# Kernel optimization log

Measured on AMD Instinct MI355X. Metric: run time of the kernel, lower is better.

The kernel has to match this reference:

```python
import jax, jax.numpy as jnp
import numpy as np
import math

P = 256   # state_dim
H = 1024  # hidden_dim
B = 8     # batch
L = 4096  # sequence length
R_MIN, R_MAX, THETA_MAX = 0.9, 0.999, math.pi


def _map_theta_to_A(thetas, G_diag, steps):
    cos_t = jnp.cos(thetas)
    tan_sq = jnp.tan(thetas) ** 2
    sqrt_term = 4.0 * jnp.sqrt(steps ** 4 / cos_t ** 2 + steps ** 5 * G_diag / cos_t ** 2)
    common = steps ** 2 * (-4.0 - 2.0 * steps * G_diag - 4.0 * tan_sq - 2.0 * steps * G_diag * tan_sq)
    denom = 2.0 * steps ** 4 * (1.0 + tan_sq)
    A_plus = (sqrt_term - common) / denom
    A_minus = (-sqrt_term - common) / denom
    return jnp.where(thetas > math.pi / 2, A_plus, A_minus)


def setup_inputs() -> dict:
    key = jax.random.key(0)
    k1, k2, k3, k4, k5, k6, k7 = jax.random.split(key, 7)
    x = jax.random.normal(k1, (B, L, H), dtype=jnp.float32)
    steps_raw = 0.5 * jax.random.normal(k2, (P,), dtype=jnp.float32)
    steps = jax.nn.sigmoid(steps_raw)
    mags = jnp.sqrt(jax.random.uniform(k3, (P,)) * (R_MAX ** 2 - R_MIN ** 2) + R_MIN ** 2)
    G_raw = (1.0 - mags ** 2) / (steps * mags ** 2)
    theta = jax.random.uniform(k4, (P,)) * THETA_MAX
    A_raw = _map_theta_to_A(theta, jax.nn.relu(G_raw), steps)
    std_b = 1.0 / math.sqrt(H)
    B_mat = jax.random.uniform(k5, (P, H, 2), minval=-std_b, maxval=std_b, dtype=jnp.float32)
    std_c = 1.0 / math.sqrt(P)
    C_mat = jax.random.uniform(k6, (H, P, 2), minval=-std_c, maxval=std_c, dtype=jnp.float32)
    D_vec = jax.random.normal(k7, (H,), dtype=jnp.float32)
    return {"input_sequence": x, "steps_raw": steps_raw, "G_raw": G_raw,
            "A_raw": A_raw, "B_mat": B_mat, "C_mat": C_mat, "D_vec": D_vec}


def _binary_operator(q_i, q_j):
    """Compose (M, F) pairs: (Mj@Mi, Mj@Fi + Fj); M flattened as [M11,M12,M21,M22] (4P)."""
    A_i, b_i = q_i
    A_j, b_j = q_j
    iA, iB, iC, iD = jnp.split(A_i, 4, axis=-1)
    jA, jB, jC, jD = jnp.split(A_j, 4, axis=-1)
    A_new = jnp.concatenate([jA * iA + jB * iC, jA * iB + jB * iD,
                             jC * iA + jD * iC, jC * iB + jD * iD], axis=-1)
    b_i1, b_i2 = jnp.split(b_i, 2, axis=-2)  # (..., P, 2) each
    new_b1 = jA[..., None] * b_i1 + jB[..., None] * b_i2
    new_b2 = jC[..., None] * b_i1 + jD[..., None] * b_i2
    return A_new, jnp.concatenate([new_b1, new_b2], axis=-2) + b_j


def _forward(x, steps_raw, G_raw, A_raw, B_mat, C_mat, D_vec):
    steps = jax.nn.sigmoid(steps_raw)          # (P,)
    G_diag = jax.nn.relu(G_raw)
    A_diag = jax.nn.relu(A_raw)

    Bu = jnp.einsum('blh,pht->blpt', x, B_mat)  # (B, L, P, 2)

    S = 1.0 + steps * G_diag                    # (P,)
    alpha = steps ** 2 * A_diag / S
    alpha = 1.99 * jnp.tanh(alpha / 1.99)
    M = jnp.concatenate([1.0 / S, -alpha / steps, steps / S, 1.0 - alpha])  # (4P,)
    M_exp = jnp.broadcast_to(M, (x.shape[0], x.shape[1], 4 * steps.shape[0]))

    step_b = steps[None, None, :, None]
    S_b = S[None, None, :, None]
    F1 = step_b * (1.0 / S_b) * Bu
    F2 = step_b ** 2 * (1.0 / S_b) * Bu
    F_mat = jnp.concatenate([F1, F2], axis=-2)  # (B, L, 2P, 2)

    _, xs = jax.lax.associative_scan(_binary_operator, (M_exp, F_mat), axis=1)
    ys = xs[..., steps.shape[0]:, :]            # (B, L, P, 2) -- the x-states

    Cy = jnp.einsum('blpt,hpt->blht', ys, C_mat)  # (B, L, H, 2)
    return Cy[..., 0] - Cy[..., 1] + x * D_vec


def reference(input_sequence, steps_raw, G_raw, A_raw, B_mat, C_mat, D_vec):
    return _forward(input_sequence, steps_raw, G_raw, A_raw, B_mat, C_mat, D_vec)
```

## Files before the change

### kernel.cpp

```cpp
#include <hip/hip_runtime.h>
#include <math.h>
#include <stdint.h>

#define PCH 256
#define HD  1024
#define BB  8
#define LL  4096
#define NN  512
#define MROWS (BB*LL)
#define NCH 64
#define TCH 64

typedef __bf16 bf16x8 __attribute__((ext_vector_type(8)));
typedef float  f32x4  __attribute__((ext_vector_type(4)));
typedef short  s16x8  __attribute__((ext_vector_type(8)));

#define OFFB_W1    ((size_t)0)
#define OFFB_C2    (OFFB_W1  + (size_t)NN*HD*2)
#define OFFB_CST   (OFFB_C2  + (size_t)HD*NN*2)
#define OFFB_BU    (OFFB_CST + (size_t)16384)
#define OFFB_YS    (OFFB_BU  + (size_t)MROWS*NN*2)
#define OFFB_ZEND  (OFFB_YS  + (size_t)MROWS*NN*2)
#define OFFB_CARRY (OFFB_ZEND + (size_t)BB*NCH*2*NN*4)

__device__ __forceinline__ short f2bf(float f) {
    union { float f; uint32_t u; } v; v.f = f;
    uint32_t r = v.u + 0x7FFFu + ((v.u >> 16) & 1u);
    return (short)(r >> 16);
}
__device__ __forceinline__ float bf2f(unsigned short u) {
    union { uint32_t u; float f; } v; v.u = ((uint32_t)u) << 16;
    return v.f;
}

__global__ void prep_consts(const float* __restrict__ steps_raw,
                            const float* __restrict__ G_raw,
                            const float* __restrict__ A_raw,
                            float* __restrict__ cst) {
    int p = threadIdx.x;
    if (p >= PCH) return;
    float steps = 1.0f / (1.0f + expf(-steps_raw[p]));
    float G = fmaxf(G_raw[p], 0.0f);
    float A = fmaxf(A_raw[p], 0.0f);
    float S = 1.0f + steps * G;
    float alpha = steps * steps * A / S;
    alpha = 1.99f * tanhf(alpha / 1.99f);
    float m11 = 1.0f / S;
    float m12 = -alpha / steps;
    float m21 = steps / S;
    float m22 = 1.0f - alpha;
    float c1 = steps / S;
    float c2 = steps * steps / S;
    float a = 1.f, b = 0.f, c = 0.f, d = 1.f;
    for (int i = 0; i < TCH; ++i) {
        float na = m11*a + m12*c;
        float nb = m11*b + m12*d;
        float nc = m21*a + m22*c;
        float nd = m21*b + m22*d;
        a = na; b = nb; c = nc; d = nd;
    }
    cst[0*PCH+p] = m11; cst[1*PCH+p] = m12; cst[2*PCH+p] = m21; cst[3*PCH+p] = m22;
    cst[4*PCH+p] = c1;  cst[5*PCH+p] = c2;
    cst[6*PCH+p] = a;   cst[7*PCH+p] = b;   cst[8*PCH+p] = c;   cst[9*PCH+p] = d;
}

__global__ void prep_w(const float* __restrict__ B_mat,
                       const float* __restrict__ C_mat,
                       short* __restrict__ W1t,
                       short* __restrict__ C2t) {
    int idx = blockIdx.x * blockDim.x + threadIdx.x;
    if (idx >= HD * NN) return;
    {
        int n = idx >> 10;
        int h = idx & (HD - 1);
        int p = n >> 1, t = n & 1;
        W1t[idx] = f2bf(B_mat[(size_t)p * HD * 2 + (size_t)h * 2 + t]);
    }
    {
        int h = idx >> 9;
        int n = idx & (NN - 1);
        int p = n >> 1, t = n & 1;
        float sgn = (t == 0) ? 1.0f : -1.0f;
        C2t[idx] = f2bf(sgn * C_mat[(size_t)h * PCH * 2 + (size_t)p * 2 + t]);
    }
}

template <int K, int N, bool A_F32, bool OUT_BF16, bool EPI>
__global__ __launch_bounds__(256, 3)
void gemm128(const void* __restrict__ Aop, const short* __restrict__ Bt,
             void* __restrict__ Cout, const float* __restrict__ xres,
             const float* __restrict__ Dv) {
    __shared__ alignas(16) char smem[32768];
    constexpr int GX = N / 128;
    const int nwg = gridDim.x;
    const int cpx = nwg >> 3;
    const int bid = blockIdx.x;
    const int wg = (bid & 7) * cpx + (bid >> 3);
    const int by = wg / GX, bx = wg % GX;
    const int m0 = by * 128, n0 = bx * 128;

    const int tid = threadIdx.x;
    const int lane = tid & 63, w = tid >> 6;
    const int wm = w >> 1, wn = w & 1;
    const int g = lane >> 4, r16 = lane & 15;

    const short* Abf  = (const short*)Aop;
    const float* Af32 = (const float*)Aop;

    auto stageB = [&](int buf, int k0) {
        #pragma unroll
        for (int s = 0; s < 2; ++s) {
            int c = tid + s * 256;
            int row = c >> 2, q = c & 3;
            int gq = q ^ ((row >> 1) & 3);
            const short* sb = Bt + (size_t)(n0 + row) * K + k0 + gq * 8;
            __builtin_amdgcn_global_load_lds(
                (const __attribute__((address_space(1))) void*)sb,
                (__attribute__((address_space(3))) void*)(smem + buf * 16384 + 8192 + c * 16),
                16, 0, 0);
        }
    };
    auto stageAbf = [&](int buf, int k0) {
        #pragma unroll
        for (int s = 0; s < 2; ++s) {
            int c = tid + s * 256;
            int row = c >> 2, q = c & 3;
            int gq = q ^ ((row >> 1) & 3);
            const short* sa = Abf + (size_t)(m0 + row) * K + k0 + gq * 8;
            __builtin_amdgcn_global_load_lds(
                (const __attribute__((address_space(1))) void*)sa,
                (__attribute__((address_space(3))) void*)(smem + buf * 16384 + c * 16),
                16, 0, 0);
        }
    };
    f32x4 av0, av1, av2, av3;
    auto loadAf32 = [&](int k0) {
        {
            int c = tid;
            int row = c >> 2, q = c & 3;
            const f32x4* px = (const f32x4*)(Af32 + (size_t)(m0 + row) * K + k0 + q * 8);
            av0 = px[0]; av1 = px[1];
        }
        {
            int c = tid + 256;
            int row = c >> 2, q = c & 3;
            const f32x4* px = (const f32x4*)(Af32 + (size_t)(m0 + row) * K + k0 + q * 8);
            av2 = px[0]; av3 = px[1];
        }
    };
    auto writeAf32 = [&](int buf) {
        {
            int c = tid;
            int row = c >> 2, q = c & 3;
            int gq = q ^ ((row >> 1) & 3);
            s16x8 r;
            #pragma unroll
            for (int j = 0; j < 4; ++j) { r[j] = f2bf(av0[j]); r[4 + j] = f2bf(av1[j]); }
            *(s16x8*)(smem + buf * 16384 + row * 64 + gq * 16) = r;
        }
        {
            int c = tid + 256;
            int row = c >> 2, q = c & 3;
            int gq = q ^ ((row >> 1) & 3);
            s16x8 r;
            #pragma unroll
            for (int j = 0; j < 4; ++j) { r[j] = f2bf(av2[j]); r[4 + j] = f2bf(av3[j]); }
            *(s16x8*)(smem + buf * 16384 + row * 64 + gq * 16) = r;
        }
    };

    const int swzg = (g ^ ((r16 >> 1) & 3)) << 4;
    int aoff[4], boff[4];
    #pragma unroll
    for (int i = 0; i < 4; ++i)
        aoff[i] = (wm * 64 + i * 16 + r16) * 64 + swzg;
    #pragma unroll
    for (int j = 0; j < 4; ++j)
        boff[j] = 8192 + (wn * 64 + j * 16 + r16) * 64 + swzg;

    f32x4 acc[4][4];
    #pragma unroll
    for (int i = 0; i < 4; ++i)
        #pragma unroll
        for (int j = 0; j < 4; ++j) acc[i][j] = (f32x4)0.0f;

    constexpr int NT = K / 32;
    if (A_F32) { loadAf32(0); stageB(0, 0); writeAf32(0); }
    else       { stageAbf(0, 0); stageB(0, 0); }
    __syncthreads();
    int cur = 0;
    #pragma unroll 1
    for (int t = 0; t < NT; ++t) {
        if (t + 1 < NT) {
            if (A_F32) loadAf32((t + 1) * 32);
            else       stageAbf(cur ^ 1, (t + 1) * 32);
            stageB(cur ^ 1, (t + 1) * 32);
        }
        const char* base = smem + cur * 16384;
        bf16x8 af[4], bfv[4];
        #pragma unroll
        for (int i = 0; i < 4; ++i) af[i] = *(const bf16x8*)(base + aoff[i]);
        #pragma unroll
        for (int j = 0; j < 4; ++j) bfv[j] = *(const bf16x8*)(base + boff[j]);
        #pragma unroll
        for (int i = 0; i < 4; ++i)
            #pragma unroll
            for (int j = 0; j < 4; ++j)
                acc[i][j] = __builtin_amdgcn_mfma_f32_16x16x32_bf16(
                    af[i], bfv[j], acc[i][j], 0, 0, 0);
        if (A_F32 && t + 1 < NT) writeAf32(cur ^ 1);
        __syncthreads();
        cur ^= 1;
    }

    const int crow0 = m0 + wm * 64 + g * 4;
    const int ccol0 = n0 + wn * 64 + r16;
    #pragma unroll
    for (int j = 0; j < 4; ++j) {
        int col = ccol0 + j * 16;
        float dv = EPI ? Dv[col] : 0.0f;
        #pragma unroll
        for (int i = 0; i < 4; ++i) {
            #pragma unroll
            for (int r = 0; r < 4; ++r) {
                size_t idx = (size_t)(crow0 + i * 16 + r) * N + col;
                float v = acc[i][j][r];
                if (EPI) v = fmaf(xres[idx], dv, v);
                if (OUT_BF16) ((unsigned short*)Cout)[idx] = (unsigned short)f2bf(v);
                else          ((float*)Cout)[idx] = v;
            }
        }
    }
}

__global__ __launch_bounds__(512)
void scan_phase1(const unsigned short* __restrict__ Bu, const float* __restrict__ cst,
                 float* __restrict__ zend) {
    int bid = blockIdx.x;
    int b = bid / NCH, c = bid % NCH;
    int n = threadIdx.x;
    int p = n >> 1;
    float m11 = cst[0*PCH+p], m12 = cst[1*PCH+p], m21 = cst[2*PCH+p], m22 = cst[3*PCH+p];
    float c1 = cst[4*PCH+p], c2 = cst[5*PCH+p];
    float s1 = 0.f, s2 = 0.f;
    const unsigned short* bp = Bu + ((size_t)(b * LL + c * TCH)) * NN + n;
    #pragma unroll 4
    for (int i = 0; i < TCH; ++i) {
        float u = bf2f(bp[(size_t)i * NN]);
        float ns1 = fmaf(m11, s1, fmaf(m12, s2, c1 * u));
        float ns2 = fmaf(m21, s1, fmaf(m22, s2, c2 * u));
        s1 = ns1; s2 = ns2;
    }
    size_t base = ((size_t)(b * NCH + c) * 2) * NN + n;
    zend[base] = s1;
    zend[base + NN] = s2;
}

__global__ __launch_bounds__(512)
void scan_phase2(const float* __restrict__ zend, const float* __restrict__ cst,
                 float* __restrict__ carry) {
    int b = blockIdx.x;
    int n = threadIdx.x;
    int p = n >> 1;
    float a = cst[6*PCH+p], bm = cst[7*PCH+p], cmt = cst[8*PCH+p], d = cst[9*PCH+p];
    float cs1 = 0.f, cs2 = 0.f;
    for (int c = 0; c < NCH; ++c) {
        size_t base = ((size_t)(b * NCH + c) * 2) * NN + n;
        float z1 = zend[base], z2 = zend[base + NN];
        float ns1 = fmaf(a, cs1, fmaf(bm, cs2, z1));
        float ns2 = fmaf(cmt, cs1, fmaf(d, cs2, z2));
        carry[base] = ns1;
        carry[base + NN] = ns2;
        cs1 = ns1; cs2 = ns2;
    }
}

__global__ __launch_bounds__(512)
void scan_phase3(const unsigned short* __restrict__ Bu, const float* __restrict__ cst,
                 const float* __restrict__ carry, unsigned short* __restrict__ ys) {
    int bid = blockIdx.x;
    int b = bid / NCH, c = bid % NCH;
    int n = threadIdx.x;
    int p = n >> 1;
    float m11 = cst[0*PCH+p], m12 = cst[1*PCH+p], m21 = cst[2*PCH+p], m22 = cst[3*PCH+p];
    float c1 = cst[4*PCH+p], c2 = cst[5*PCH+p];
    float s1 = 0.f, s2 = 0.f;
    if (c > 0) {
        size_t base = ((size_t)(b * NCH + (c - 1)) * 2) * NN + n;
        s1 = carry[base];
        s2 = carry[base + NN];
    }
    const unsigned short* bp = Bu + ((size_t)(b * LL + c * TCH)) * NN + n;
    unsigned short* yp = ys + ((size_t)(b * LL + c * TCH)) * NN + n;
    #pragma unroll 4
    for (int i = 0; i < TCH; ++i) {
        float u = bf2f(bp[(size_t)i * NN]);
        float ns1 = fmaf(m11, s1, fmaf(m12, s2, c1 * u));
        float ns2 = fmaf(m21, s1, fmaf(m22, s2, c2 * u));
        s1 = ns1; s2 = ns2;
        yp[(size_t)i * NN] = (unsigned short)f2bf(s2);
    }
}

extern "C" void kernel_launch(void* const* d_in, const int* in_sizes, int n_in,
                              void* d_out, int out_size, void* d_ws, size_t ws_size,
                              hipStream_t stream) {
    const float* x         = (const float*)d_in[0];
    const float* steps_raw = (const float*)d_in[1];
    const float* G_raw     = (const float*)d_in[2];
    const float* A_raw     = (const float*)d_in[3];
    const float* B_mat     = (const float*)d_in[4];
    const float* C_mat     = (const float*)d_in[5];
    const float* D_vec     = (const float*)d_in[6];
    float* out = (float*)d_out;
    char*  ws  = (char*)d_ws;

    short*          W1t   = (short*)(ws + OFFB_W1);
    short*          C2t   = (short*)(ws + OFFB_C2);
    float*          cst   = (float*)(ws + OFFB_CST);
    unsigned short* Bu    = (unsigned short*)(ws + OFFB_BU);
    unsigned short* ysbf  = (unsigned short*)(ws + OFFB_YS);
    float*          zend  = (float*)(ws + OFFB_ZEND);
    float*          carry = (float*)(ws + OFFB_CARRY);

    prep_consts<<<1, 256, 0, stream>>>(steps_raw, G_raw, A_raw, cst);
    prep_w<<<(HD * NN) / 512, 512, 0, stream>>>(B_mat, C_mat, W1t, C2t);

    gemm128<HD, NN, true, true, false><<<(NN / 128) * (MROWS / 128), 256, 0, stream>>>(
        (const void*)x, W1t, (void*)Bu, nullptr, nullptr);

    scan_phase1<<<BB * NCH, 512, 0, stream>>>(Bu, cst, zend);
    scan_phase2<<<BB, 512, 0, stream>>>(zend, cst, carry);
    scan_phase3<<<BB * NCH, 512, 0, stream>>>(Bu, cst, carry, ysbf);

    gemm128<NN, HD, false, false, true><<<(HD / 128) * (MROWS / 128), 256, 0, stream>>>(
        (const void*)ysbf, C2t, (void*)out, x, D_vec);
}
```

Measured before the change: 207.2 us.

## Use 256x256 tiled bf16 GEMM with 512 threads for output projection

Splits the templated GEMM into a specialized fp32-A kernel for the input projection and a new 256x256-tile, 512-thread, BK=64 kernel for the output projection with the D-skip epilogue. Larger tiles raise arithmetic intensity and cut redundant global loads of ys and C weights. The cost is 128KB of LDS and heavier register pressure, which limits occupancy to one or two blocks per CU and leaves fewer workgroups to spread across CUs.

```diff
diff --git a/kernel.cpp b/kernel.cpp
--- a/kernel.cpp
+++ b/kernel.cpp
@@ -85,11 +85,10 @@
     }
 }
 
-template <int K, int N, bool A_F32, bool OUT_BF16, bool EPI>
+template <int K, int N>
 __global__ __launch_bounds__(256, 3)
-void gemm128(const void* __restrict__ Aop, const short* __restrict__ Bt,
-             void* __restrict__ Cout, const float* __restrict__ xres,
-             const float* __restrict__ Dv) {
+void gemm128_cvtA(const float* __restrict__ Af32, const short* __restrict__ Bt,
+                  unsigned short* __restrict__ Cout) {
     __shared__ alignas(16) char smem[32768];
     constexpr int GX = N / 128;
     const int nwg = gridDim.x;
@@ -103,9 +102,6 @@
     const int lane = tid & 63, w = tid >> 6;
     const int wm = w >> 1, wn = w & 1;
     const int g = lane >> 4, r16 = lane & 15;
-
-    const short* Abf  = (const short*)Aop;
-    const float* Af32 = (const float*)Aop;
 
     auto stageB = [&](int buf, int k0) {
         #pragma unroll
@@ -120,19 +116,6 @@
                 16, 0, 0);
         }
     };
-    auto stageAbf = [&](int buf, int k0) {
-        #pragma unroll
-        for (int s = 0; s < 2; ++s) {
-            int c = tid + s * 256;
-            int row = c >> 2, q = c & 3;
-            int gq = q ^ ((row >> 1) & 3);
-            const short* sa = Abf + (size_t)(m0 + row) * K + k0 + gq * 8;
-            __builtin_amdgcn_global_load_lds(
-                (const __attribute__((address_space(1))) void*)sa,
-                (__attribute__((address_space(3))) void*)(smem + buf * 16384 + c * 16),
-                16, 0, 0);
-        }
-    };
     f32x4 av0, av1, av2, av3;
     auto loadAf32 = [&](int k0) {
         {
@@ -185,15 +168,13 @@
         for (int j = 0; j < 4; ++j) acc[i][j] = (f32x4)0.0f;
 
     constexpr int NT = K / 32;
-    if (A_F32) { loadAf32(0); stageB(0, 0); writeAf32(0); }
-    else       { stageAbf(0, 0); stageB(0, 0); }
+    loadAf32(0); stageB(0, 0); writeAf32(0);
     __syncthreads();
     int cur = 0;
     #pragma unroll 1
     for (int t = 0; t < NT; ++t) {
         if (t + 1 < NT) {
-            if (A_F32) loadAf32((t + 1) * 32);
-            else       stageAbf(cur ^ 1, (t + 1) * 32);
+            loadAf32((t + 1) * 32);
             stageB(cur ^ 1, (t + 1) * 32);
         }
         const char* base = smem + cur * 16384;
@@ -208,7 +189,7 @@
             for (int j = 0; j < 4; ++j)
                 acc[i][j] = __builtin_amdgcn_mfma_f32_16x16x32_bf16(
                     af[i], bfv[j], acc[i][j], 0, 0, 0);
-        if (A_F32 && t + 1 < NT) writeAf32(cur ^ 1);
+        if (t + 1 < NT) writeAf32(cur ^ 1);
         __syncthreads();
         cur ^= 1;
     }
@@ -218,16 +199,121 @@
     #pragma unroll
     for (int j = 0; j < 4; ++j) {
         int col = ccol0 + j * 16;
-        float dv = EPI ? Dv[col] : 0.0f;
         #pragma unroll
         for (int i = 0; i < 4; ++i) {
             #pragma unroll
             for (int r = 0; r < 4; ++r) {
                 size_t idx = (size_t)(crow0 + i * 16 + r) * N + col;
-                float v = acc[i][j][r];
+                Cout[idx] = (unsigned short)f2bf(acc[i][j][r]);
+            }
+        }
+    }
+}
+
+template <int K, int N, bool EPI>
+__global__ __launch_bounds__(512, 2)
+void gemm256(const short* __restrict__ A, const short* __restrict__ Bt,
+             float* __restrict__ Cout, const float* __restrict__ xres,
+             const float* __restrict__ Dv) {
+    __shared__ alignas(16) char smem[131072];
+    constexpr int GX = N / 256;
+    const int nwg = gridDim.x;
+    const int cpx = nwg >> 3;
+    const int bid = blockIdx.x;
+    const int wg = (bid & 7) * cpx + (bid >> 3);
+    const int by = wg / GX, bx = wg % GX;
+    const int m0 = by * 256, n0 = bx * 256;
+
+    const int tid = threadIdx.x;
+    const int lane = tid & 63, w = tid >> 6;
+    const int wm = w >> 2, wn = w & 3;
+    const int g = lane >> 4, r16 = lane & 15;
+
+    auto stage = [&](int buf, int k0) {
+        #pragma unroll
+        for (int s = 0; s < 4; ++s) {
+            int c = tid + s * 512;
+            int row = c >> 3, q = c & 7;
+            int gq = q ^ (row & 7);
+            const short* sa = A + (size_t)(m0 + row) * K + k0 + gq * 8;
+            __builtin_amdgcn_global_load_lds(
+                (const __attribute__((address_space(1))) void*)sa,
+                (__attribute__((address_space(3))) void*)(smem + buf * 65536 + c * 16),
+                16, 0, 0);
+        }
+        #pragma unroll
+        for (int s = 0; s < 4; ++s) {
+            int c = tid + s * 512;
+            int row = c >> 3, q = c & 7;
+            int gq = q ^ (row & 7);
+            const short* sb = Bt + (size_t)(n0 + row) * K + k0 + gq * 8;
+            __builtin_amdgcn_global_load_lds(
+                (const __attribute__((address_space(1))) void*)sb,
+                (__attribute__((address_space(3))) void*)(smem + buf * 65536 + 32768 + c * 16),
+                16, 0, 0);
+        }
+    };
+
+    int aoff[8], boff[4];
+    #pragma unroll
+    for (int mi = 0; mi < 8; ++mi) {
+        int ra = wm * 128 + mi * 16 + r16;
+        aoff[mi] = ra * 128 + ((g ^ (ra & 7)) << 4);
+    }
+    #pragma unroll
+    for (int nj = 0; nj < 4; ++nj) {
+        int rb = wn * 64 + nj * 16 + r16;
+        boff[nj] = 32768 + rb * 128 + ((g ^ (rb & 7)) << 4);
+    }
+
+    f32x4 acc[8][4];
+    #pragma unroll
+    for (int mi = 0; mi < 8; ++mi)
+        #pragma unroll
+        for (int nj = 0; nj < 4; ++nj) acc[mi][nj] = (f32x4)0.0f;
+
+    constexpr int NT = K / 64;
+    stage(0, 0);
+    __syncthreads();
+    int cur = 0;
+    #pragma unroll 1
+    for (int t = 0; t < NT; ++t) {
+        if (t + 1 < NT) stage(cur ^ 1, (t + 1) * 64);
+        const char* base = smem + cur * 65536;
+        #pragma unroll
+        for (int kk = 0; kk < 2; ++kk) {
+            bf16x8 af[8], bfv[4];
+            #pragma unroll
+            for (int mi = 0; mi < 8; ++mi)
+                af[mi] = *(const bf16x8*)(base + (aoff[mi] ^ (kk << 6)));
+            #pragma unroll
+            for (int nj = 0; nj < 4; ++nj)
+                bfv[nj] = *(const bf16x8*)(base + (boff[nj] ^ (kk << 6)));
+            #pragma unroll
+            for (int mi = 0; mi < 8; ++mi)
+                #pragma unroll
+                for (int nj = 0; nj < 4; ++nj)
+                    acc[mi][nj] = __builtin_amdgcn_mfma_f32_16x16x32_bf16(
+                        af[mi], bfv[nj], acc[mi][nj], 0, 0, 0);
+        }
+        __syncthreads();
+        cur ^= 1;
+    }
+
+    const int crow0 = m0 + wm * 128 + g * 4;
+    const int ccol0 = n0 + wn * 64 + r16;
+    #pragma unroll
+    for (int nj = 0; nj < 4; ++nj) {
+        int col = ccol0 + nj * 16;
+        float dv = EPI ? Dv[col] : 0.0f;
+        #pragma unroll
+        for (int mi = 0; mi < 8; ++mi) {
+            #pragma unroll
+            for (int r = 0; r < 4; ++r) {
+                size_t idx = (size_t)(crow0 + mi * 16 + r) * N + col;
+                float v = acc[mi][nj][r];
                 if (EPI) v = fmaf(xres[idx], dv, v);
-                if (OUT_BF16) ((unsigned short*)Cout)[idx] = (unsigned short)f2bf(v);
-                else          ((float*)Cout)[idx] = v;
+                Cout[idx] = v;
             }
         }
     }
@@ -326,13 +412,13 @@
     prep_consts<<<1, 256, 0, stream>>>(steps_raw, G_raw, A_raw, cst);
     prep_w<<<(HD * NN) / 512, 512, 0, stream>>>(B_mat, C_mat, W1t, C2t);
 
-    gemm128<HD, NN, true, true, false><<<(NN / 128) * (MROWS / 128), 256, 0, stream>>>(
-        (const void*)x, W1t, (void*)Bu, nullptr, nullptr);
+    gemm128_cvtA<HD, NN><<<(NN / 128) * (MROWS / 128), 256, 0, stream>>>(
+        x, W1t, Bu);
 
     scan_phase1<<<BB * NCH, 512, 0, stream>>>(Bu, cst, zend);
     scan_phase2<<<BB, 512, 0, stream>>>(zend, cst, carry);
     scan_phase3<<<BB * NCH, 512, 0, stream>>>(Bu, cst, carry, ysbf);
 
-    gemm128<NN, HD, false, false, true><<<(HD / 128) * (MROWS / 128), 256, 0, stream>>>(
-        (const void*)ysbf, C2t, (void*)out, x, D_vec);
-}
+    gemm256<NN, HD, true><<<(HD / 256) * (MROWS / 256), 512, 0, stream>>>(
+        (const short*)ysbf, C2t, out, x, D_vec);
+}
```

Measured after the change: 199.1 us. 1.04x faster.
